# Performance work log

Measured on AMD Instinct MI355X. Metric: run time of the kernel, lower is better.

## Reference

```python
import jax, jax.numpy as jnp
import numpy as np

DIM = 256
NUM_HEADS = 4
KEY_DIM = 16
ATTN_RATIO = 2
D = ATTN_RATIO * KEY_DIM  # 32
WS = 7
QKV_DIM = NUM_HEADS * KEY_DIM * 2 + NUM_HEADS * D  # 256
SCALE = KEY_DIM ** -0.5


def setup_inputs() -> dict:
    key = jax.random.key(0)
    k1, k2, k3 = jax.random.split(key, 3)
    x = jax.random.normal(k1, (32, DIM, 112, 112), jnp.float32)
    # Linear weights stored as [in, out] so y = x @ W + b (same math as torch's x @ W.T)
    Wqkv = jax.random.normal(k2, (DIM, QKV_DIM), jnp.float32) * 0.05
    bqkv = jnp.zeros((QKV_DIM,), jnp.float32)
    Wproj = jax.random.normal(k3, (NUM_HEADS * D, DIM), jnp.float32) * 0.05
    bproj = jnp.zeros((DIM,), jnp.float32)
    return {"x": x, "Wqkv": Wqkv, "bqkv": bqkv, "Wproj": Wproj, "bproj": bproj}


def reference(x, Wqkv, bqkv, Wproj, bproj):
    B, C, H, W = x.shape
    ws = WS
    pad_h = (ws - H % ws) % ws
    pad_w = (ws - W % ws) % ws
    xp = jnp.pad(x, ((0, 0), (0, 0), (0, pad_h), (0, pad_w)))
    Hp, Wp = H + pad_h, W + pad_w
    nwh, nww = Hp // ws, Wp // ws
    N = ws * ws  # tokens per window (49)
    # window partition: (B, C, nwh, ws, nww, ws) -> (B*nwh*nww, N, C)
    xw = xp.reshape(B, C, nwh, ws, nww, ws).transpose(0, 2, 4, 3, 5, 1)
    xw = xw.reshape(B * nwh * nww, N, C)
    # tiny multi-head attention within each window
    qkv = xw @ Wqkv + bqkv  # [Bw, N, QKV_DIM]
    qt = NUM_HEADS * KEY_DIM
    q = qkv[:, :, :qt].reshape(-1, N, NUM_HEADS, KEY_DIM).transpose(0, 2, 1, 3)
    k = qkv[:, :, qt:2 * qt].reshape(-1, N, NUM_HEADS, KEY_DIM).transpose(0, 2, 1, 3)
    v = qkv[:, :, 2 * qt:].reshape(-1, N, NUM_HEADS, D).transpose(0, 2, 1, 3)
    attn = jax.nn.softmax(jnp.einsum('bhnd,bhmd->bhnm', q, k) * SCALE, axis=-1)
    o = jnp.einsum('bhnm,bhmd->bhnd', attn, v)  # [Bw, H, N, D]
    o = o.transpose(0, 2, 1, 3).reshape(-1, N, NUM_HEADS * D)
    o = o @ Wproj + bproj  # [Bw, N, C]
    # window merge: reverse of the partition
    o = o.reshape(B, nwh, nww, ws, ws, C).transpose(0, 5, 1, 3, 2, 4)
    o = o.reshape(B, C, Hp, Wp)
    return o[:, :, :H, :W]
```

## Files before the change

### kernel.cpp

```cpp
#include <hip/hip_runtime.h>
#include <hip/hip_bf16.h>


typedef short bf16x8 __attribute__((ext_vector_type(8)));
typedef float f32x4 __attribute__((ext_vector_type(4)));

static __device__ __forceinline__ unsigned short cvt1(float f) {
    __hip_bfloat16 h = __float2bfloat16(f);
    unsigned short u; __builtin_memcpy(&u, &h, 2); return u;
}
static __device__ __forceinline__ unsigned int cvt2(float a, float b) {
    float2 t; t.x = a; t.y = b;
    __hip_bfloat162 h = __float22bfloat162_rn(t);
    unsigned int u; __builtin_memcpy(&u, &h, 4); return u;
}
static __device__ __forceinline__ float bf2f(unsigned int hs) {
    return __uint_as_float(hs << 16);
}

#define WQ_ELEMS 65536LL
#define WP_ELEMS 32768LL

__global__ void prep_weights(const float* __restrict__ Wqkv,
                             const float* __restrict__ Wproj,
                             unsigned short* __restrict__ wq,
                             unsigned short* __restrict__ wp) {
    int tid = blockIdx.x * 256 + threadIdx.x;
    if (tid < 8192) {
        int lane = tid & 63, f = tid >> 6;
        int kt = f & 7, nt = f >> 3;
        int kbase = kt * 32 + (lane >> 4) * 8;
        int col = nt * 16 + (lane & 15);
        uint4 u;
        u.x = cvt2(Wqkv[(kbase + 0) * 256 + col], Wqkv[(kbase + 1) * 256 + col]);
        u.y = cvt2(Wqkv[(kbase + 2) * 256 + col], Wqkv[(kbase + 3) * 256 + col]);
        u.z = cvt2(Wqkv[(kbase + 4) * 256 + col], Wqkv[(kbase + 5) * 256 + col]);
        u.w = cvt2(Wqkv[(kbase + 6) * 256 + col], Wqkv[(kbase + 7) * 256 + col]);
        *reinterpret_cast<uint4*>(&wq[(long long)tid * 8]) = u;
    } else if (tid < 12288) {
        int i2 = tid - 8192;
        int lane = i2 & 63, f = i2 >> 6;
        int kt = f & 3, nt = f >> 2;
        int kbase = kt * 32 + (lane >> 4) * 8;
        int col = nt * 16 + (lane & 15);
        uint4 u;
        u.x = cvt2(Wproj[(kbase + 0) * 256 + col], Wproj[(kbase + 1) * 256 + col]);
        u.y = cvt2(Wproj[(kbase + 2) * 256 + col], Wproj[(kbase + 3) * 256 + col]);
        u.z = cvt2(Wproj[(kbase + 4) * 256 + col], Wproj[(kbase + 5) * 256 + col]);
        u.w = cvt2(Wproj[(kbase + 6) * 256 + col], Wproj[(kbase + 7) * 256 + col]);
        *reinterpret_cast<uint4*>(&wp[(long long)i2 * 8]) = u;
    }
}


__global__ __launch_bounds__(256, 3) void win_attn(
    const float* __restrict__ x,
    const unsigned short* __restrict__ wfq,
    const unsigned short* __restrict__ wfp,
    const float* __restrict__ bqkv,
    const float* __restrict__ bproj,
    float* __restrict__ out)
{
    __shared__ __align__(16) unsigned short A[16384];

    const int tid  = threadIdx.x;
    const int lane = tid & 63;
    const int wave = tid >> 6;
    const int lr   = lane & 15;
    const int kg   = lane >> 4;

    const int bid = (int)blockIdx.x;
    const int L   = (bid & 7) * 1024 + (bid >> 3);
    const int b   = L >> 8;
    const int rem = L & 255;
    const int h0 = (rem >> 4) * 7;
    const int w0 = (rem & 15) * 7;
    const int xwin = (b * 256) * 12544 + h0 * 112 + w0;

    float bqv[4], bpv[4];
    #pragma unroll
    for (int nn = 0; nn < 4; ++nn) {
        bqv[nn] = bqkv[wave * 64 + nn * 16 + lr];
        bpv[nn] = bproj[wave * 64 + nn * 16 + lr];
    }

    {
        uint4 z4 = uint4{0u, 0u, 0u, 0u};
        #pragma unroll
        for (int i = 0; i < 2; ++i)
            reinterpret_cast<uint4*>(&A[49 * 256])[tid + i * 256] = z4;
    }

    if (lane < 49) {
        const int lb = xwin + (lane / 7) * 112 + (lane % 7);
        #pragma unroll 4
        for (int it = 0; it < 16; ++it) {
            const int c0 = wave * 64 + it * 4;
            const float v0 = x[lb + (c0 + 0) * 12544];
            const float v1 = x[lb + (c0 + 1) * 12544];
            const float v2 = x[lb + (c0 + 2) * 12544];
            const float v3 = x[lb + (c0 + 3) * 12544];
            uint2 pk; pk.x = cvt2(v0, v1); pk.y = cvt2(v2, v3);
            const int e = lane * 256 + (((c0 >> 3) ^ (lane & 7)) << 3) + (c0 & 7);
            *reinterpret_cast<uint2*>(&A[e]) = pk;
        }
    }
    __syncthreads();

    f32x4 acc[4][4];
    #pragma unroll
    for (int m = 0; m < 4; ++m)
        #pragma unroll
        for (int nn = 0; nn < 4; ++nn)
            acc[m][nn] = f32x4{0.f, 0.f, 0.f, 0.f};

    #pragma unroll
    for (int kt = 0; kt < 8; ++kt) {
        bf16x8 a[4], bw[4];
        #pragma unroll
        for (int m = 0; m < 4; ++m) {
            const int row = lr + 16 * m;
            const int ch  = (kt * 4 + kg) ^ (row & 7);
            a[m] = *reinterpret_cast<const bf16x8*>(&A[row * 256 + ch * 8]);
        }
        #pragma unroll
        for (int nn = 0; nn < 4; ++nn) {
            const int nt = wave * 4 + nn;
            bw[nn] = *reinterpret_cast<const bf16x8*>(&wfq[((nt * 8 + kt) * 64 + lane) * 8]);
        }
        #pragma unroll
        for (int m = 0; m < 4; ++m)
            #pragma unroll
            for (int nn = 0; nn < 4; ++nn)
                acc[m][nn] = __builtin_amdgcn_mfma_f32_16x16x32_bf16(a[m], bw[nn], acc[m][nn], 0, 0, 0);
    }
    __syncthreads();

    #pragma unroll
    for (int nn = 0; nn < 4; ++nn) {
        const int colg = wave * 64 + nn * 16 + lr;
        #pragma unroll
        for (int m = 0; m < 4; ++m)
            #pragma unroll
            for (int r = 0; r < 4; ++r) {
                const int row = kg * 4 + r + 16 * m;
                const unsigned short hv = cvt1(acc[m][nn][r] + bqv[nn]);
                if (wave < 2) {
                    const int c = colg & 63;
                    A[(wave << 12) + row * 64 + (((c >> 3) ^ (row & 7)) << 3) + (c & 7)] = hv;
                } else {
                    const int vc = colg - 128;
                    const int hh = vc >> 5, d = vc & 31;
                    A[8192 + hh * 2048 + d * 64 + (((row >> 3) ^ (d & 7)) << 3) + (row & 7)] = hv;
                }
            }
    }
    __syncthreads();

    const int h = wave;
    const bf16x8 zf = {0, 0, 0, 0, 0, 0, 0, 0};

    bf16x8 kf[4];
    #pragma unroll
    for (int km = 0; km < 4; ++km) {
        if (lane < 32) {
            const int row = lr + 16 * km;
            kf[km] = *reinterpret_cast<const bf16x8*>(
                &A[4096 + row * 64 + (((h * 2 + kg) ^ (row & 7)) << 3)]);
        } else kf[km] = zf;
    }
    bf16x8 vb[2][2];
    #pragma unroll
    for (int kt = 0; kt < 2; ++kt)
        #pragma unroll
        for (int nt = 0; nt < 2; ++nt) {
            const int d = lr + 16 * nt;
            const int ch = (kt * 4 + kg) ^ (d & 7);
            vb[kt][nt] = *reinterpret_cast<const bf16x8*>(&A[8192 + h * 2048 + d * 64 + ch * 8]);
        }

    const int a0 = (((kg & 1) * 2)     * 16 + lr) * 4;
    const int a1 = (((kg & 1) * 2 + 1) * 16 + lr) * 4;

    f32x4 oacc[4][2];
    #pragma unroll
    for (int qn = 0; qn < 4; ++qn) {
        oacc[qn][0] = f32x4{0.f, 0.f, 0.f, 0.f};
        oacc[qn][1] = f32x4{0.f, 0.f, 0.f, 0.f};
    }
    const float C = 0.25f * 1.44269504f;

    #pragma unroll
    for (int qn = 0; qn < 4; ++qn) {
        bf16x8 qf;
        if (lane < 32) {
            const int row = lr + 16 * qn;
            qf = *reinterpret_cast<const bf16x8*>(
                &A[row * 64 + (((h * 2 + kg) ^ (row & 7)) << 3)]);
        } else qf = zf;

        f32x4 s[4];
        #pragma unroll
        for (int km = 0; km < 4; ++km) {
            f32x4 z = f32x4{0.f, 0.f, 0.f, 0.f};
            s[km] = __builtin_amdgcn_mfma_f32_16x16x32_bf16(kf[km], qf, z, 0, 0, 0);
        }

        float e[4][4];
        float sum = 0.f;
        #pragma unroll
        for (int km = 0; km < 4; ++km)
            #pragma unroll
            for (int r = 0; r < 4; ++r) {
                float v = __builtin_amdgcn_exp2f(s[km][r] * C);
                if (km == 3 && !(kg == 0 && r == 0)) v = 0.f;
                e[km][r] = v;
                sum += v;
            }
        sum += __shfl_xor(sum, 16, 64);
        sum += __shfl_xor(sum, 32, 64);
        const float rs = __builtin_amdgcn_rcpf(sum);

        unsigned int D[4][2];
        #pragma unroll
        for (int km = 0; km < 4; ++km) {
            D[km][0] = cvt2(e[km][0] * rs, e[km][1] * rs);
            D[km][1] = cvt2(e[km][2] * rs, e[km][3] * rs);
        }

        #pragma unroll
        for (int kt = 0; kt < 2; ++kt) {
            const int klo = 2 * kt, khi = 2 * kt + 1;
            const unsigned int t0 = (unsigned)__builtin_amdgcn_ds_bpermute(a0, (int)D[klo][0]);
            const unsigned int u0 = (unsigned)__builtin_amdgcn_ds_bpermute(a0, (int)D[khi][0]);
            const unsigned int t1 = (unsigned)__builtin_amdgcn_ds_bpermute(a0, (int)D[klo][1]);
            const unsigned int u1 = (unsigned)__builtin_amdgcn_ds_bpermute(a0, (int)D[khi][1]);
            const unsigned int t2 = (unsigned)__builtin_amdgcn_ds_bpermute(a1, (int)D[klo][0]);
            const unsigned int u2 = (unsigned)__builtin_amdgcn_ds_bpermute(a1, (int)D[khi][0]);
            const unsigned int t3 = (unsigned)__builtin_amdgcn_ds_bpermute(a1, (int)D[klo][1]);
            const unsigned int u3 = (unsigned)__builtin_amdgcn_ds_bpermute(a1, (int)D[khi][1]);
            union { unsigned int u[4]; bf16x8 v; } pu;
            pu.u[0] = (kg < 2) ? t0 : u0;
            pu.u[1] = (kg < 2) ? t1 : u1;
            pu.u[2] = (kg < 2) ? t2 : u2;
            pu.u[3] = (kg < 2) ? t3 : u3;
            oacc[qn][0] = __builtin_amdgcn_mfma_f32_16x16x32_bf16(pu.v, vb[kt][0], oacc[qn][0], 0, 0, 0);
            oacc[qn][1] = __builtin_amdgcn_mfma_f32_16x16x32_bf16(pu.v, vb[kt][1], oacc[qn][1], 0, 0, 0);
        }
    }

    __syncthreads();

    #pragma unroll
    for (int qn = 0; qn < 4; ++qn)
        #pragma unroll
        for (int nt = 0; nt < 2; ++nt)
            #pragma unroll
            for (int r = 0; r < 4; ++r) {
                const int row = kg * 4 + r + 16 * qn;
                const int col = h * 32 + nt * 16 + lr;
                A[row * 128 + (((col >> 3) ^ (row & 7)) << 3) + (col & 7)] =
                    cvt1(oacc[qn][nt][r]);
            }
    __syncthreads();

    f32x4 pc[4][4];
    #pragma unroll
    for (int m = 0; m < 4; ++m)
        #pragma unroll
        for (int nn = 0; nn < 4; ++nn)
            pc[m][nn] = f32x4{0.f, 0.f, 0.f, 0.f};

    #pragma unroll
    for (int kt = 0; kt < 4; ++kt) {
        bf16x8 a[4], bw[4];
        #pragma unroll
        for (int m = 0; m < 4; ++m) {
            const int row = lr + 16 * m;
            const int ch = (kt * 4 + kg) ^ (row & 7);
            a[m] = *reinterpret_cast<const bf16x8*>(&A[row * 128 + ch * 8]);
        }
        #pragma unroll
        for (int nn = 0; nn < 4; ++nn) {
            const int nt = wave * 4 + nn;
            bw[nn] = *reinterpret_cast<const bf16x8*>(&wfp[((nt * 4 + kt) * 64 + lane) * 8]);
        }
        #pragma unroll
        for (int m = 0; m < 4; ++m)
            #pragma unroll
            for (int nn = 0; nn < 4; ++nn)
                pc[m][nn] = __builtin_amdgcn_mfma_f32_16x16x32_bf16(a[m], bw[nn], pc[m][nn], 0, 0, 0);
    }
    __syncthreads();

    #pragma unroll
    for (int nn = 0; nn < 4; ++nn) {
        const int colg = wave * 64 + nn * 16 + lr;
        #pragma unroll
        for (int m = 0; m < 4; ++m)
            #pragma unroll
            for (int r = 0; r < 4; ++r) {
                const int row = kg * 4 + r + 16 * m;
                A[row * 256 + (((colg >> 3) ^ (row & 7)) << 3) + (colg & 7)] = cvt1(pc[m][nn][r] + bpv[nn]);
            }
    }
    __builtin_amdgcn_wave_barrier();

    if (lane < 49) {
        const int lb = xwin + (lane / 7) * 112 + (lane % 7);
        #pragma unroll 4
        for (int it = 0; it < 16; ++it) {
            const int c0 = wave * 64 + it * 4;
            const int e = lane * 256 + (((c0 >> 3) ^ (lane & 7)) << 3) + (c0 & 7);
            const uint2 pk = *reinterpret_cast<const uint2*>(&A[e]);
            out[lb + (c0 + 0) * 12544] = bf2f(pk.x & 0xffffu);
            out[lb + (c0 + 1) * 12544] = bf2f(pk.x >> 16);
            out[lb + (c0 + 2) * 12544] = bf2f(pk.y & 0xffffu);
            out[lb + (c0 + 3) * 12544] = bf2f(pk.y >> 16);
        }
    }
}

extern "C" void kernel_launch(void* const* d_in, const int* in_sizes, int n_in,
                              void* d_out, int out_size, void* d_ws, size_t ws_size,
                              hipStream_t stream) {
    const float* x     = (const float*)d_in[0];
    const float* Wqkv  = (const float*)d_in[1];
    const float* bqkv  = (const float*)d_in[2];
    const float* Wproj = (const float*)d_in[3];
    const float* bproj = (const float*)d_in[4];
    float* out = (float*)d_out;

    unsigned short* wfq = (unsigned short*)d_ws;
    unsigned short* wfp = wfq + WQ_ELEMS;

    prep_weights<<<48, 256, 0, stream>>>(Wqkv, Wproj, wfq, wfp);
    win_attn<<<8192, 256, 16384, stream>>>(x, wfq, wfp, bqkv, bproj, out);
}
```

Measured before the change: 386.5 us.

## Swap MFMA operand order so accumulators pack into vectorized LDS stores

The QKV, PV and projection MFMAs now swap their A/B operands wherever that places four contiguous output elements in each lane. The epilogues can then write packed uint2 bf16 stores into swizzled LDS instead of scalar 16-bit stores, which cuts LDS store instructions and bank traffic. Biases are loaded as float4 to match the transposed layout. Softmax normalization is deferred by scaling the PV output by the reciprocal sum rather than scaling the probabilities first, which slightly changes where bf16 rounding happens.

```diff
diff --git a/kernel.cpp b/kernel.cpp
--- a/kernel.cpp
+++ b/kernel.cpp
@@ -68,6 +68,7 @@
     const int wave = tid >> 6;
     const int lr   = lane & 15;
     const int kg   = lane >> 4;
+    const bool qkw = (wave < 2);
 
     const int bid = (int)blockIdx.x;
     const int L   = (bid & 7) * 1024 + (bid >> 3);
@@ -77,11 +78,12 @@
     const int w0 = (rem & 15) * 7;
     const int xwin = (b * 256) * 12544 + h0 * 112 + w0;
 
-    float bqv[4], bpv[4];
-    #pragma unroll
-    for (int nn = 0; nn < 4; ++nn) {
-        bqv[nn] = bqkv[wave * 64 + nn * 16 + lr];
-        bpv[nn] = bproj[wave * 64 + nn * 16 + lr];
+    float4 bq4[4]; float bqs[4]; float4 bp4[4];
+    #pragma unroll
+    for (int i = 0; i < 4; ++i) {
+        if (qkw) bq4[i] = *reinterpret_cast<const float4*>(&bqkv[wave * 64 + i * 16 + kg * 4]);
+        else     bqs[i] = bqkv[wave * 64 + i * 16 + lr];
+        bp4[i] = *reinterpret_cast<const float4*>(&bproj[wave * 64 + i * 16 + kg * 4]);
     }
 
     {
@@ -90,7 +92,6 @@
         for (int i = 0; i < 2; ++i)
             reinterpret_cast<uint4*>(&A[49 * 256])[tid + i * 256] = z4;
     }
-
     if (lane < 49) {
         const int lb = xwin + (lane / 7) * 112 + (lane % 7);
         #pragma unroll 4
@@ -128,32 +129,53 @@
             const int nt = wave * 4 + nn;
             bw[nn] = *reinterpret_cast<const bf16x8*>(&wfq[((nt * 8 + kt) * 64 + lane) * 8]);
         }
-        #pragma unroll
-        for (int m = 0; m < 4; ++m)
-            #pragma unroll
-            for (int nn = 0; nn < 4; ++nn)
-                acc[m][nn] = __builtin_amdgcn_mfma_f32_16x16x32_bf16(a[m], bw[nn], acc[m][nn], 0, 0, 0);
-    }
-    __syncthreads();
-
-    #pragma unroll
-    for (int nn = 0; nn < 4; ++nn) {
-        const int colg = wave * 64 + nn * 16 + lr;
-        #pragma unroll
-        for (int m = 0; m < 4; ++m)
-            #pragma unroll
-            for (int r = 0; r < 4; ++r) {
-                const int row = kg * 4 + r + 16 * m;
-                const unsigned short hv = cvt1(acc[m][nn][r] + bqv[nn]);
-                if (wave < 2) {
-                    const int c = colg & 63;
-                    A[(wave << 12) + row * 64 + (((c >> 3) ^ (row & 7)) << 3) + (c & 7)] = hv;
-                } else {
-                    const int vc = colg - 128;
-                    const int hh = vc >> 5, d = vc & 31;
-                    A[8192 + hh * 2048 + d * 64 + (((row >> 3) ^ (d & 7)) << 3) + (row & 7)] = hv;
-                }
+        if (qkw) {
+            #pragma unroll
+            for (int ci = 0; ci < 4; ++ci)
+                #pragma unroll
+                for (int tj = 0; tj < 4; ++tj)
+                    acc[ci][tj] = __builtin_amdgcn_mfma_f32_16x16x32_bf16(bw[ci], a[tj], acc[ci][tj], 0, 0, 0);
+        } else {
+            #pragma unroll
+            for (int tm = 0; tm < 4; ++tm)
+                #pragma unroll
+                for (int cn = 0; cn < 4; ++cn)
+                    acc[tm][cn] = __builtin_amdgcn_mfma_f32_16x16x32_bf16(a[tm], bw[cn], acc[tm][cn], 0, 0, 0);
+        }
+    }
+    __syncthreads();
+
+    if (qkw) {
+        #pragma unroll
+        for (int ci = 0; ci < 4; ++ci) {
+            const int cch = ci * 2 + (kg >> 1);
+            const int clo = (kg & 1) * 4;
+            #pragma unroll
+            for (int tj = 0; tj < 4; ++tj) {
+                const int tok = tj * 16 + lr;
+                uint2 pk;
+                pk.x = cvt2(acc[ci][tj][0] + bq4[ci].x, acc[ci][tj][1] + bq4[ci].y);
+                pk.y = cvt2(acc[ci][tj][2] + bq4[ci].z, acc[ci][tj][3] + bq4[ci].w);
+                *reinterpret_cast<uint2*>(
+                    &A[(wave << 12) + tok * 64 + ((cch ^ (tok & 7)) << 3) + clo]) = pk;
             }
+        }
+    } else {
+        #pragma unroll
+        for (int cn = 0; cn < 4; ++cn) {
+            const int vc = wave * 64 + cn * 16 + lr - 128;
+            const int hh = vc >> 5, d = vc & 31;
+            #pragma unroll
+            for (int tm = 0; tm < 4; ++tm) {
+                const int tch = tm * 2 + (kg >> 1);
+                const int tlo = (kg & 1) * 4;
+                uint2 pk;
+                pk.x = cvt2(acc[tm][cn][0] + bqs[cn], acc[tm][cn][1] + bqs[cn]);
+                pk.y = cvt2(acc[tm][cn][2] + bqs[cn], acc[tm][cn][3] + bqs[cn]);
+                *reinterpret_cast<uint2*>(
+                    &A[8192 + hh * 2048 + d * 64 + ((tch ^ (d & 7)) << 3) + tlo]) = pk;
+            }
+        }
     }
     __syncthreads();
 
@@ -188,6 +210,7 @@
         oacc[qn][0] = f32x4{0.f, 0.f, 0.f, 0.f};
         oacc[qn][1] = f32x4{0.f, 0.f, 0.f, 0.f};
     }
+    float rsv[4];
     const float C = 0.25f * 1.44269504f;
 
     #pragma unroll
@@ -217,16 +240,15 @@
                 e[km][r] = v;
                 sum += v;
             }
+        unsigned int D[4][2];
+        #pragma unroll
+        for (int km = 0; km < 4; ++km) {
+            D[km][0] = cvt2(e[km][0], e[km][1]);
+            D[km][1] = cvt2(e[km][2], e[km][3]);
+        }
         sum += __shfl_xor(sum, 16, 64);
         sum += __shfl_xor(sum, 32, 64);
-        const float rs = __builtin_amdgcn_rcpf(sum);
-
-        unsigned int D[4][2];
-        #pragma unroll
-        for (int km = 0; km < 4; ++km) {
-            D[km][0] = cvt2(e[km][0] * rs, e[km][1] * rs);
-            D[km][1] = cvt2(e[km][2] * rs, e[km][3] * rs);
-        }
+        rsv[qn] = __builtin_amdgcn_rcpf(sum);
 
         #pragma unroll
         for (int kt = 0; kt < 2; ++kt) {
@@ -244,24 +266,28 @@
             pu.u[1] = (kg < 2) ? t1 : u1;
             pu.u[2] = (kg < 2) ? t2 : u2;
             pu.u[3] = (kg < 2) ? t3 : u3;
-            oacc[qn][0] = __builtin_amdgcn_mfma_f32_16x16x32_bf16(pu.v, vb[kt][0], oacc[qn][0], 0, 0, 0);
-            oacc[qn][1] = __builtin_amdgcn_mfma_f32_16x16x32_bf16(pu.v, vb[kt][1], oacc[qn][1], 0, 0, 0);
-        }
-    }
-
-    __syncthreads();
-
-    #pragma unroll
-    for (int qn = 0; qn < 4; ++qn)
-        #pragma unroll
-        for (int nt = 0; nt < 2; ++nt)
-            #pragma unroll
-            for (int r = 0; r < 4; ++r) {
-                const int row = kg * 4 + r + 16 * qn;
-                const int col = h * 32 + nt * 16 + lr;
-                A[row * 128 + (((col >> 3) ^ (row & 7)) << 3) + (col & 7)] =
-                    cvt1(oacc[qn][nt][r]);
-            }
+            oacc[qn][0] = __builtin_amdgcn_mfma_f32_16x16x32_bf16(vb[kt][0], pu.v, oacc[qn][0], 0, 0, 0);
+            oacc[qn][1] = __builtin_amdgcn_mfma_f32_16x16x32_bf16(vb[kt][1], pu.v, oacc[qn][1], 0, 0, 0);
+        }
+    }
+
+    __syncthreads();
+
+    #pragma unroll
+    for (int qn = 0; qn < 4; ++qn) {
+        const float rs = rsv[qn];
+        const int tok = qn * 16 + lr;
+        #pragma unroll
+        for (int nt = 0; nt < 2; ++nt) {
+            const int cch = h * 4 + nt * 2 + (kg >> 1);
+            const int clo = (kg & 1) * 4;
+            uint2 pk;
+            pk.x = cvt2(oacc[qn][nt][0] * rs, oacc[qn][nt][1] * rs);
+            pk.y = cvt2(oacc[qn][nt][2] * rs, oacc[qn][nt][3] * rs);
+            *reinterpret_cast<uint2*>(
+                &A[tok * 128 + ((cch ^ (tok & 7)) << 3) + clo]) = pk;
+        }
+    }
     __syncthreads();
 
     f32x4 pc[4][4];
@@ -275,34 +301,37 @@
     for (int kt = 0; kt < 4; ++kt) {
         bf16x8 a[4], bw[4];
         #pragma unroll
-        for (int m = 0; m < 4; ++m) {
-            const int row = lr + 16 * m;
+        for (int tj = 0; tj < 4; ++tj) {
+            const int row = lr + 16 * tj;
             const int ch = (kt * 4 + kg) ^ (row & 7);
-            a[m] = *reinterpret_cast<const bf16x8*>(&A[row * 128 + ch * 8]);
-        }
-        #pragma unroll
-        for (int nn = 0; nn < 4; ++nn) {
-            const int nt = wave * 4 + nn;
-            bw[nn] = *reinterpret_cast<const bf16x8*>(&wfp[((nt * 4 + kt) * 64 + lane) * 8]);
-        }
-        #pragma unroll
-        for (int m = 0; m < 4; ++m)
-            #pragma unroll
-            for (int nn = 0; nn < 4; ++nn)
-                pc[m][nn] = __builtin_amdgcn_mfma_f32_16x16x32_bf16(a[m], bw[nn], pc[m][nn], 0, 0, 0);
-    }
-    __syncthreads();
-
-    #pragma unroll
-    for (int nn = 0; nn < 4; ++nn) {
-        const int colg = wave * 64 + nn * 16 + lr;
-        #pragma unroll
-        for (int m = 0; m < 4; ++m)
-            #pragma unroll
-            for (int r = 0; r < 4; ++r) {
-                const int row = kg * 4 + r + 16 * m;
-                A[row * 256 + (((colg >> 3) ^ (row & 7)) << 3) + (colg & 7)] = cvt1(pc[m][nn][r] + bpv[nn]);
-            }
+            a[tj] = *reinterpret_cast<const bf16x8*>(&A[row * 128 + ch * 8]);
+        }
+        #pragma unroll
+        for (int ci = 0; ci < 4; ++ci) {
+            const int nt = wave * 4 + ci;
+            bw[ci] = *reinterpret_cast<const bf16x8*>(&wfp[((nt * 4 + kt) * 64 + lane) * 8]);
+        }
+        #pragma unroll
+        for (int ci = 0; ci < 4; ++ci)
+            #pragma unroll
+            for (int tj = 0; tj < 4; ++tj)
+                pc[ci][tj] = __builtin_amdgcn_mfma_f32_16x16x32_bf16(bw[ci], a[tj], pc[ci][tj], 0, 0, 0);
+    }
+    __syncthreads();
+
+    #pragma unroll
+    for (int ci = 0; ci < 4; ++ci) {
+        const int cch = wave * 8 + ci * 2 + (kg >> 1);
+        const int clo = (kg & 1) * 4;
+        #pragma unroll
+        for (int tj = 0; tj < 4; ++tj) {
+            const int tok = tj * 16 + lr;
+            uint2 pk;
+            pk.x = cvt2(pc[ci][tj][0] + bp4[ci].x, pc[ci][tj][1] + bp4[ci].y);
+            pk.y = cvt2(pc[ci][tj][2] + bp4[ci].z, pc[ci][tj][3] + bp4[ci].w);
+            *reinterpret_cast<uint2*>(
+                &A[tok * 256 + ((cch ^ (tok & 7)) << 3) + clo]) = pk;
+        }
     }
     __builtin_amdgcn_wave_barrier();
 
```

After: 515.1 us. 33.3% more time.

## Synchronize blocks per image row-band before output stores via global counters

Applied to the files above, without the earlier changes.

Adds a templated mode in which each block increments a global per-band counter and spins, with a bounded poll count, until all 16 windows of its row band arrive, then stores output. The aim is to make the blocks writing one 7-row band store together so the strided NCHW output writes coalesce better in cache and DRAM. It adds a memset, atomics and spin-waiting, and the wait can stall if co-resident blocks are not scheduled. It also changes the zero-fill of the LDS padding rows to cover the whole tail region.

```diff
diff --git a/kernel.cpp b/kernel.cpp
--- a/kernel.cpp
+++ b/kernel.cpp
@@ -20,6 +20,8 @@
 
 #define WQ_ELEMS 65536LL
 #define WP_ELEMS 32768LL
+#define CNT_OFF  ((WQ_ELEMS + WP_ELEMS) * 2)
+#define WS_NEED  (CNT_OFF + 512 * 4)
 
 __global__ void prep_weights(const float* __restrict__ Wqkv,
                              const float* __restrict__ Wproj,
@@ -53,13 +55,15 @@
 }
 
 
+template <int STORM>
 __global__ __launch_bounds__(256, 3) void win_attn(
     const float* __restrict__ x,
     const unsigned short* __restrict__ wfq,
     const unsigned short* __restrict__ wfp,
     const float* __restrict__ bqkv,
     const float* __restrict__ bproj,
-    float* __restrict__ out)
+    float* __restrict__ out,
+    unsigned int* __restrict__ cnt)
 {
     __shared__ __align__(16) unsigned short A[16384];
 
@@ -86,11 +90,9 @@
 
     {
         uint4 z4 = uint4{0u, 0u, 0u, 0u};
-        #pragma unroll
-        for (int i = 0; i < 2; ++i)
-            reinterpret_cast<uint4*>(&A[49 * 256])[tid + i * 256] = z4;
-    }
-
+        for (int i = tid; i < 480; i += 256)
+            reinterpret_cast<uint4*>(&A[49 * 256])[i] = z4;
+    }
     if (lane < 49) {
         const int lb = xwin + (lane / 7) * 112 + (lane % 7);
         #pragma unroll 4
@@ -304,7 +306,19 @@
                 A[row * 256 + (((colg >> 3) ^ (row & 7)) << 3) + (colg & 7)] = cvt1(pc[m][nn][r] + bpv[nn]);
             }
     }
-    __builtin_amdgcn_wave_barrier();
+
+    if constexpr (STORM) {
+        __syncthreads();
+        if (tid == 0) {
+            const int band = L >> 4;
+            atomicAdd(&cnt[band], 1u);
+            int polls = 0;
+            while (polls < 400 && atomicAdd(&cnt[band], 0u) < 16u) ++polls;
+        }
+        __syncthreads();
+    } else {
+        __builtin_amdgcn_wave_barrier();
+    }
 
     if (lane < 49) {
         const int lb = xwin + (lane / 7) * 112 + (lane % 7);
@@ -335,5 +349,12 @@
     unsigned short* wfp = wfq + WQ_ELEMS;
 
     prep_weights<<<48, 256, 0, stream>>>(Wqkv, Wproj, wfq, wfp);
-    win_attn<<<8192, 256, 16384, stream>>>(x, wfq, wfp, bqkv, bproj, out);
-}
+
+    if (ws_size >= (size_t)WS_NEED) {
+        unsigned int* cnt = (unsigned int*)((char*)d_ws + CNT_OFF);
+        hipMemsetAsync(cnt, 0, 512 * sizeof(unsigned int), stream);
+        win_attn<1><<<8192, 256, 16384, stream>>>(x, wfq, wfp, bqkv, bproj, out, cnt);
+    } else {
+        win_attn<0><<<8192, 256, 16384, stream>>>(x, wfq, wfp, bqkv, bproj, out, nullptr);
+    }
+}
```

New measurement: 489.8 us. +26.7%, slower.
